# Kernel tuning notes

Measured on AMD Instinct MI355X. Metric: run time of the kernel, lower is better.

Reference implementation:

```python
import jax, jax.numpy as jnp
import numpy as np

N_DOC, N_WORD, N_ENT, N_POS = 10000, 20000, 10000, 60
D, D_POS_IN, D_WEMB = 128, 60, 300
E11, E22, E33, E01, E02, E03 = 320000, 160000, 3600, 300000, 100000, 150000
EPS = 1e-9


def spmm(rows, cols, vals, x, n_out):
    """Sparse (n_out x n_in) adjacency @ x via gather + weighted segment-sum."""
    return jax.ops.segment_sum(vals[:, None] * x[cols], rows, num_segments=n_out)


def gcn(rows, cols, vals, x, n_out, W=None, b=None):
    """GCN layer: adj @ (x W + b) with ReLU; identity=True in torch == W is None."""
    h = x if W is None else x @ W + b
    return jax.nn.relu(spmm(rows, cols, vals, h, n_out))


def setup_inputs():
    key = jax.random.key(0)
    ks = iter(jax.random.split(key, 64))
    randn = lambda s: jax.random.normal(next(ks), s, jnp.float32)
    rand = lambda s: jax.random.uniform(next(ks), s, dtype=jnp.float32)
    ridx = lambda s, hi: jax.random.randint(next(ks), s, 0, hi, jnp.int32)
    return {
        "f1": randn((N_WORD, D)),
        "f2": randn((N_ENT, D)),
        "f3": randn((N_POS, D_POS_IN)),
        "word_emb": randn((N_ENT, D_WEMB)),
        "a11_rows": ridx((E11,), N_WORD), "a11_cols": ridx((E11,), N_WORD), "a11_vals": rand((E11,)),
        "a22_rows": ridx((E22,), N_ENT), "a22_cols": ridx((E22,), N_ENT), "a22_vals": rand((E22,)),
        "a33_rows": ridx((E33,), N_POS), "a33_cols": ridx((E33,), N_POS), "a33_vals": rand((E33,)),
        "a01_rows": ridx((E01,), N_DOC), "a01_cols": ridx((E01,), N_WORD), "a01_vals": rand((E01,)),
        "a02_rows": ridx((E02,), N_DOC), "a02_cols": ridx((E02,), N_ENT), "a02_vals": rand((E02,)),
        "a03_rows": ridx((E03,), N_DOC), "a03_cols": ridx((E03,), N_POS), "a03_vals": rand((E03,)),
        "W3": randn((D_POS_IN, D)) * 0.1, "b3": jnp.zeros((D,), jnp.float32),
        "W1_2": randn((D, D)) * 0.1, "b1_2": jnp.zeros((D,), jnp.float32),
        "W2_2": randn((D, D)) * 0.1, "b2_2": jnp.zeros((D,), jnp.float32),
        "W3_2": randn((D, D)) * 0.1, "b3_2": jnp.zeros((D,), jnp.float32),
    }


def reference(f1, f2, f3, word_emb,
              a11_rows, a11_cols, a11_vals, a22_rows, a22_cols, a22_vals,
              a33_rows, a33_cols, a33_vals, a01_rows, a01_cols, a01_vals,
              a02_rows, a02_cols, a02_vals, a03_rows, a03_cols, a03_vals,
              W3, b3, W1_2, b1_2, W2_2, b2_2, W3_2, b3_2):
    # eval mode: F.dropout(training=False) is a no-op
    # type 1 (words): GCN(identity=True) -> GCN_2
    h1 = gcn(a11_rows, a11_cols, a11_vals, f1, N_WORD)
    h1 = gcn(a11_rows, a11_cols, a11_vals, h1, N_WORD, W1_2, b1_2)
    # type 2 (entities, concat_word_emb=True): GCN(identity=True) -> GCN_2 -> concat word_emb
    h2 = gcn(a22_rows, a22_cols, a22_vals, f2, N_ENT)
    h2 = gcn(a22_rows, a22_cols, a22_vals, h2, N_ENT, W2_2, b2_2)
    h2 = jnp.concatenate([h2, word_emb], axis=-1)  # [N_ENT, D + D_WEMB]
    # type 3 (POS): full GCN -> GCN_2
    h3 = gcn(a33_rows, a33_cols, a33_vals, f3, N_POS, W3, b3)
    h3 = gcn(a33_rows, a33_cols, a33_vals, h3, N_POS, W3_2, b3_2)
    # cross-type aggregation onto documents + L2 normalization
    outs = []
    for rows, cols, vals, h in ((a01_rows, a01_cols, a01_vals, h1),
                                (a02_rows, a02_cols, a02_vals, h2),
                                (a03_rows, a03_cols, a03_vals, h3)):
        agg = spmm(rows, cols, vals, h, N_DOC)  # [N_DOC, d]
        outs.append(agg / (jnp.linalg.norm(agg, axis=-1, keepdims=True) + EPS))
    return tuple(outs)
```

## Files before the change

kernel.cpp:

```cpp
#include <hip/hip_runtime.h>
#include <hip/hip_bf16.h>

typedef __hip_bfloat16 bf16;

#define N_DOC   10000
#define N_WORD  20000
#define N_ENT   10000
#define N_POS   60
#define DD      128
#define D_WEMB  300
#define E11     320000
#define E22     160000
#define E33     3600
#define E01     300000
#define E02     100000
#define E03     150000

#define ROFF11  0
#define ROFF22  20000
#define ROFF33  30000
#define ROFF01  30060
#define ROFF02  40060
#define ROFF03  50060
#define NROWS   60060
#define EOFF11  0
#define EOFF22  320000
#define EOFF33  480000
#define EOFF01  483600
#define EOFF02  783600
#define EOFF03  883600
#define NEDGES  1033600

#define BSHIFT  9
#define NBUCK   118
#define BCAP    18432
#define P1_TILE 4096
#define P1_EPT  8

#define BFO_F1B     0
#define BFO_F2B     1280000
#define BFO_WEMBB   1920000
#define BFO_E0B     3420000
#define BFO_S0B     4349952
#define BFO_S1B     5629952
#define BFO_E1B     6909952
#define BFO_P3A     7549952
#define BFO_P3B     7557632
#define BFO_INT     7565312

__device__ __forceinline__ float loadf(const void* p, size_t i, int isb) {
    return isb ? __bfloat162float(((const bf16*)p)[i])
               : ((const float*)p)[i];
}
__device__ __forceinline__ float b2f(unsigned u16) {
    union { unsigned v; float f; } x; x.v = u16 << 16; return x.f;
}
__device__ __forceinline__ unsigned f2b(float f) {
    bf16 h = __float2bfloat16(f);
    union { bf16 h; unsigned short u; } x; x.h = h; return (unsigned)x.u;
}
__device__ __forceinline__ void storef(void* p, size_t i, int asb, float v) {
    if (asb) ((unsigned short*)p)[i] = (unsigned short)f2b(v);
    else     ((float*)p)[i] = v;
}
__device__ __forceinline__ unsigned pack_pair(int col, float v) {
    return (f2b(v) << 16) | (unsigned)col;
}

__device__ __forceinline__ void edge_decode(
        int i,
        const int* __restrict__ r11, const int* __restrict__ c11, const void* __restrict__ v11,
        const int* __restrict__ r22, const int* __restrict__ c22, const void* __restrict__ v22,
        const int* __restrict__ r33, const int* __restrict__ c33, const void* __restrict__ v33,
        const int* __restrict__ r01, const int* __restrict__ c01, const void* __restrict__ v01,
        const int* __restrict__ r02, const int* __restrict__ c02, const void* __restrict__ v02,
        const int* __restrict__ r03, const int* __restrict__ c03, const void* __restrict__ v03,
        int isb, int& slot, int& col, float& val) {
    if      (i < EOFF22) { int k = i;          slot = ROFF11 + r11[k]; col = c11[k]; val = loadf(v11, k, isb); }
    else if (i < EOFF33) { int k = i - EOFF22; slot = ROFF22 + r22[k]; col = c22[k]; val = loadf(v22, k, isb); }
    else if (i < EOFF01) { int k = i - EOFF33; slot = ROFF33 + r33[k]; col = c33[k]; val = loadf(v33, k, isb); }
    else if (i < EOFF02) { int k = i - EOFF01; slot = ROFF01 + r01[k]; col = c01[k]; val = loadf(v01, k, isb); }
    else if (i < EOFF03) { int k = i - EOFF02; slot = ROFF02 + r02[k]; col = c02[k]; val = loadf(v02, k, isb); }
    else                 { int k = i - EOFF03; slot = ROFF03 + r03[k]; col = c03[k]; val = loadf(v03, k, isb); }
}

__global__ void detect_kernel(const unsigned* __restrict__ probe, int* __restrict__ flag,
                              int* __restrict__ bcur) {
    __shared__ int cnt;
    if (threadIdx.x == 0) cnt = 0;
    __syncthreads();
    int insane = 0;
    for (int i = threadIdx.x; i < 1024; i += 256) {
        float x = __uint_as_float(probe[i]);
        float a = fabsf(x);
        if (!(a > 1e-10f && a < 1e10f)) insane++;
    }
    atomicAdd(&cnt, insane);
    if (bcur && threadIdx.x < NBUCK) bcur[threadIdx.x] = threadIdx.x * BCAP;
    __syncthreads();
    if (threadIdx.x == 0) *flag = (cnt > 512) ? 1 : 0;
}

__device__ __forceinline__ void conv_seg(const void* __restrict__ src,
                                         unsigned* __restrict__ dst,
                                         int npairs, int isb, int tid, int stride) {
    if (isb) {
        const unsigned* s = (const unsigned*)src;
        for (int i = tid; i < npairs; i += stride) dst[i] = s[i];
    } else {
        const float2* s = (const float2*)src;
        for (int i = tid; i < npairs; i += stride) {
            float2 x = s[i];
            dst[i] = f2b(x.x) | (f2b(x.y) << 16);
        }
    }
}
__global__ void convert_bf16(const void* __restrict__ f1, const void* __restrict__ f2,
                             const void* __restrict__ wemb,
                             unsigned* __restrict__ f1b, unsigned* __restrict__ f2b,
                             unsigned* __restrict__ wembB,
                             const int* __restrict__ dflag) {
    int isb = *dflag;
    int tid = blockIdx.x * blockDim.x + threadIdx.x;
    int stride = gridDim.x * blockDim.x;
    conv_seg(f1,   f1b,   N_WORD * (DD / 2),     isb, tid, stride);
    conv_seg(f2,   f2b,   N_ENT  * (DD / 2),     isb, tid, stride);
    conv_seg(wemb, wembB, N_ENT  * (D_WEMB / 2), isb, tid, stride);
}

__global__ __launch_bounds__(512) void bin_edges(
        const int* __restrict__ r11, const int* __restrict__ c11, const void* __restrict__ v11,
        const int* __restrict__ r22, const int* __restrict__ c22, const void* __restrict__ v22,
        const int* __restrict__ r33, const int* __restrict__ c33, const void* __restrict__ v33,
        const int* __restrict__ r01, const int* __restrict__ c01, const void* __restrict__ v01,
        const int* __restrict__ r02, const int* __restrict__ c02, const void* __restrict__ v02,
        const int* __restrict__ r03, const int* __restrict__ c03, const void* __restrict__ v03,
        int* __restrict__ bcur, uint2* __restrict__ staging,
        const int* __restrict__ dflag) {
    __shared__ int hist[NBUCK], gbase[NBUCK], cursor[NBUCK];
    int t = threadIdx.x;
    if (t < NBUCK) { hist[t] = 0; cursor[t] = 0; }
    __syncthreads();
    int isb = *dflag;
    int base0 = blockIdx.x * P1_TILE;
    unsigned rx[P1_EPT], ry[P1_EPT];
    int bk[P1_EPT];
    #pragma unroll
    for (int k = 0; k < P1_EPT; ++k) {
        int i = base0 + t + k * 512;
        bk[k] = -1;
        if (i < NEDGES) {
            int slot, col; float val;
            edge_decode(i, r11, c11, v11, r22, c22, v22, r33, c33, v33,
                        r01, c01, v01, r02, c02, v02, r03, c03, v03,
                        isb, slot, col, val);
            rx[k] = ((unsigned)slot << 16) | (unsigned)col;
            ry[k] = f2b(val);
            bk[k] = slot >> BSHIFT;
            atomicAdd(&hist[bk[k]], 1);
        }
    }
    __syncthreads();
    if (t < NBUCK) {
        int c = hist[t];
        gbase[t] = c ? atomicAdd(bcur + t, c) : 0;
    }
    __syncthreads();
    #pragma unroll
    for (int k = 0; k < P1_EPT; ++k) {
        if (bk[k] >= 0) {
            int p = atomicAdd(&cursor[bk[k]], 1);
            int dst = gbase[bk[k]] + p;
            if (dst < (bk[k] + 1) * BCAP)
                staging[dst] = make_uint2(rx[k], ry[k]);
        }
    }
}

__global__ void scan_buckets(const int* __restrict__ bcur, int* __restrict__ bbase,
                             int* __restrict__ G) {
    __shared__ int wtop[2];
    int t = threadIdx.x;
    int cnt = 0;
    if (t < NBUCK) {
        int c = bcur[t] - t * BCAP;
        cnt = (c < BCAP) ? c : BCAP;
    }
    int lane = t & 63, w = t >> 6;
    int s = cnt;
    #pragma unroll
    for (int off = 1; off < 64; off <<= 1) {
        int y = __shfl_up(s, off);
        if (lane >= off) s += y;
    }
    if (lane == 63) wtop[w] = s;
    __syncthreads();
    int woff = (w > 0) ? wtop[0] : 0;
    if (t < NBUCK) bbase[t] = woff + s - cnt;
    if (t == NBUCK - 1) { bbase[NBUCK] = woff + s; G[NROWS] = woff + s; }
}

__global__ __launch_bounds__(512) void finalize_csr(
        const int* __restrict__ bcur, const int* __restrict__ bbase,
        const uint2* __restrict__ staging,
        int* __restrict__ G, unsigned* __restrict__ pairs) {
    __shared__ int h[512], rp[512], cu[512];
    __shared__ int wsum2[8];
    int b = blockIdx.x, t = threadIdx.x;
    int cnt = bcur[b] - b * BCAP;
    if (cnt > BCAP) cnt = BCAP;
    int bb = bbase[b];
    h[t] = 0;
    __syncthreads();
    const uint2* st = staging + (size_t)b * BCAP;
    for (int i = t; i < cnt; i += 512)
        atomicAdd(&h[(st[i].x >> 16) & 511], 1);
    __syncthreads();
    int lane = t & 63, w = t >> 6;
    int x = h[t];
    int s = x;
    #pragma unroll
    for (int off = 1; off < 64; off <<= 1) {
        int y = __shfl_up(s, off);
        if (lane >= off) s += y;
    }
    if (lane == 63) wsum2[w] = s;
    __syncthreads();
    if (t < 8) {
        int v = wsum2[t];
        #pragma unroll
        for (int off = 1; off < 8; off <<= 1) {
            int y = __shfl_up(v, off);
            if (lane >= off) v += y;
        }
        wsum2[t] = v;
    }
    __syncthreads();
    int myrp = ((w > 0) ? wsum2[w - 1] : 0) + s - x;
    rp[t] = myrp;
    cu[t] = 0;
    int slot = (b << BSHIFT) + t;
    if (slot < NROWS) G[slot] = bb + myrp;
    __syncthreads();
    for (int i = t; i < cnt; i += 512) {
        uint2 r = st[i];
        int sl = (r.x >> 16) & 511;
        int p = atomicAdd(&cu[sl], 1);
        pairs[bb + rp[sl] + p] = (r.y << 16) | (r.x & 0xffffu);
    }
}

__global__ void hist2_kernel(const int* __restrict__ rowsA, int nEA,
                             const int* __restrict__ rowsB, int nEB,
                             int nA, int* __restrict__ cnt) {
    int i = blockIdx.x * blockDim.x + threadIdx.x;
    if (i < nEA) atomicAdd(cnt + rowsA[i], 1);
    else if (i < nEA + nEB) atomicAdd(cnt + nA + rowsB[i - nEA], 1);
}

__device__ void scan_ex(const int* __restrict__ cnt, int* __restrict__ rp, int n) {
    __shared__ int wsum[16];
    __shared__ int carry;
    int t = threadIdx.x, lane = t & 63, w = t >> 6;
    if (t == 0) carry = 0;
    __syncthreads();
    for (int base = 0; base < n; base += 1024) {
        int i = base + t;
        int x = (i < n) ? cnt[i] : 0;
        int s = x;
        #pragma unroll
        for (int off = 1; off < 64; off <<= 1) {
            int y = __shfl_up(s, off);
            if (lane >= off) s += y;
        }
        if (lane == 63) wsum[w] = s;
        __syncthreads();
        if (w == 0) {
            int v = (lane < 16) ? wsum[lane] : 0;
            #pragma unroll
            for (int off = 1; off < 16; off <<= 1) {
                int y = __shfl_up(v, off);
                if (lane >= off) v += y;
            }
            if (lane < 16) wsum[lane] = v;
        }
        __syncthreads();
        int woff = (w > 0) ? wsum[w - 1] : 0;
        if (i < n) rp[i] = carry + woff + s - x;
        __syncthreads();
        if (t == 0) carry += wsum[15];
        __syncthreads();
    }
    if (t == 0) rp[n] = carry;
}

__global__ __launch_bounds__(1024) void scan2_kernel(
        const int* __restrict__ cntA, int* __restrict__ rpA, int nA,
        const int* __restrict__ cntB, int* __restrict__ rpB, int nB) {
    scan_ex(cntA, rpA, nA);
    __syncthreads();
    scan_ex(cntB, rpB, nB);
}

// ... 234 lines not shown
                int pi = lane + 64 * s;
                if (pi < P2) {
                    float2 x = s0p[pi], y = s1p[pi];
                    a2[s].x  = fmaf(v0, x.x, a2[s].x);
                    a2[s].y  = fmaf(v0, x.y, a2[s].y);
                    b2v[s].x = fmaf(v1, y.x, b2v[s].x);
                    b2v[s].y = fmaf(v1, y.y, b2v[s].y);
                }
            }
        }
    }
    if (e < e1) {
        unsigned pp = pairs[e];
        int c = pp & 0xffffu;
        float v = b2f(pp >> 16);
        float x0, x1;
        if (s1b) {
            unsigned u = ((const unsigned*)((const bf16*)src1 + (size_t)c * DD))[lane];
            x0 = b2f(u & 0xffffu); x1 = b2f(u >> 16);
        } else {
            float2 x = ((const float2*)((const float*)src1 + (size_t)c * DD))[lane];
            x0 = x.x; x1 = x.y;
        }
        x0 = fmaxf(x0, 0.f); x1 = fmaxf(x1, 0.f);
        a1.x = fmaf(v, x0, a1.x); a1.y = fmaf(v, x1, a1.y);
        if (s2b) {
            const unsigned* sp = (const unsigned*)((const bf16*)src2 + (size_t)c * D_WEMB);
            #pragma unroll
            for (int s = 0; s < 3; ++s) {
                int pi = lane + 64 * s;
                if (pi < P2) {
                    unsigned u = sp[pi];
                    a2[s].x = fmaf(v, b2f(u & 0xffffu), a2[s].x);
                    a2[s].y = fmaf(v, b2f(u >> 16),     a2[s].y);
                }
            }
        } else {
            const float2* sp = (const float2*)((const float*)src2 + (size_t)c * D_WEMB);
            #pragma unroll
            for (int s = 0; s < 3; ++s) {
                int pi = lane + 64 * s;
                if (pi < P2) {
                    float2 x = sp[pi];
                    a2[s].x = fmaf(v, x.x, a2[s].x);
                    a2[s].y = fmaf(v, x.y, a2[s].y);
                }
            }
        }
    }
    float t1x = a1.x + b1.x, t1y = a1.y + b1.y;
    float t2x[3], t2y[3];
    #pragma unroll
    for (int s = 0; s < 3; ++s) { t2x[s] = a2[s].x + b2v[s].x; t2y[s] = a2[s].y + b2v[s].y; }
    float ss = t1x * t1x + t1y * t1y;
    #pragma unroll
    for (int s = 0; s < 3; ++s) {
        int pi = lane + 64 * s;
        if (pi < P2) ss += t2x[s] * t2x[s] + t2y[s] * t2y[s];
    }
    #pragma unroll
    for (int off = 32; off > 0; off >>= 1) ss += __shfl_down(ss, off);
    ss = __shfl(ss, 0);
    float inv = 1.0f / (sqrtf(ss) + 1e-9f);
    size_t base = elem_off + (size_t)row * (DD + D_WEMB);
    if (isb) {
        ((unsigned*)((bf16*)out + base))[lane] = f2b(t1x * inv) | (f2b(t1y * inv) << 16);
        unsigned* o2 = (unsigned*)((bf16*)out + base + DD);
        #pragma unroll
        for (int s = 0; s < 3; ++s) {
            int pi = lane + 64 * s;
            if (pi < P2) o2[pi] = f2b(t2x[s] * inv) | (f2b(t2y[s] * inv) << 16);
        }
    } else {
        ((float2*)((float*)out + base))[lane] = make_float2(t1x * inv, t1y * inv);
        float2* o2 = (float2*)((float*)out + base + DD);
        #pragma unroll
        for (int s = 0; s < 3; ++s) {
            int pi = lane + 64 * s;
            if (pi < P2) o2[pi] = make_float2(t2x[s] * inv, t2y[s] * inv);
        }
    }
}

template<bool RELU, int K>
__device__ __forceinline__ void rowpar_body256(
        const void* __restrict__ X, int xisb,
        const void* __restrict__ W, const void* __restrict__ b,
        void* __restrict__ out, int oisb, int isb,
        int row, int tid, float* xr ) {
    int half = tid >> 7;
    int j = tid & 127;
    float* xrh = xr + half * K;
    if (j < K) {
        float x = loadf(X, (size_t)row * K + j, xisb);
        if (RELU) x = fmaxf(x, 0.f);
        xrh[j] = x;
    }
    __syncthreads();
    float acc = loadf(b, j, isb);
    #pragma unroll 8
    for (int k = 0; k < K; ++k)
        acc = fmaf(xrh[k], loadf(W, (size_t)k * 128 + j, isb), acc);
    storef(out, (size_t)row * 128 + j, oisb, acc);
}

template<bool RELU>
__global__ void spmm_gather128(const int* __restrict__ rowptr, const unsigned* __restrict__ pairs,
                               const void* __restrict__ src, int src_flagged,
                               void* __restrict__ dst, int dst_flagged,
                               int n, const int* __restrict__ dflag) {
    int row = blockIdx.x * 4 + (threadIdx.x >> 6);
    if (row >= n) return;
    int isb = *dflag;
    gather128_body<RELU>(rowptr, pairs, src, src_flagged ? isb : 0,
                         dst, dst_flagged ? isb : 0, row, threadIdx.x & 63);
}

template<int KP, bool PRELU>
__global__ void hop_pos(const int* __restrict__ G, const unsigned* __restrict__ pairs,
                        int roff1, const void* __restrict__ src1, void* __restrict__ dst1, int n1, int B1,
                        int roff2, const void* __restrict__ src2, void* __restrict__ dst2, int n2, int B2,
                        const void* __restrict__ PX, const void* __restrict__ PW,
                        const void* __restrict__ Pb, void* __restrict__ PO,
                        const int* __restrict__ dflag) {
    __shared__ float xr[2 * KP];
    int b = blockIdx.x;
    if (b < B1) {
        int row = b * 4 + (threadIdx.x >> 6);
        if (row >= n1) return;
        gather128_body<false>(G + roff1, pairs, src1, 1, dst1, 1, row, threadIdx.x & 63);
    } else if (b < B1 + B2) {
        int row = (b - B1) * 4 + (threadIdx.x >> 6);
        if (row >= n2) return;
        gather128_body<false>(G + roff2, pairs, src2, 1, dst2, 1, row, threadIdx.x & 63);
    } else {
        int isb = *dflag;
        int row = (b - B1 - B2) * 2 + (threadIdx.x >> 7);
        if (row >= N_POS) return;
        rowpar_body256<PRELU, KP>(PX, isb, PW, Pb, PO, isb, isb, row, threadIdx.x, xr);
    }
}

template<bool RELU>
__global__ void spmm_norm128(const int* __restrict__ rowptr, const unsigned* __restrict__ pairs,
                             const void* __restrict__ src, int src_flagged,
                             void* __restrict__ out, size_t elem_off,
                             int n, const int* __restrict__ dflag) {
    int row = blockIdx.x * 4 + (threadIdx.x >> 6);
    if (row >= n) return;
    int isb = *dflag;
    norm128_body<RELU>(rowptr, pairs, src, src_flagged ? isb : 0, out, elem_off,
                       row, threadIdx.x & 63, isb);
}

__global__ void spmm2_norm(const int* __restrict__ rowptr, const unsigned* __restrict__ pairs,
                           const void* __restrict__ src1, int s1_flagged,
                           const void* __restrict__ src2, int s2_flagged,
                           void* __restrict__ out, size_t elem_off,
                           int n, const int* __restrict__ dflag) {
    int row = blockIdx.x * 4 + (threadIdx.x >> 6);
    if (row >= n) return;
    int isb = *dflag;
    norm428_body(rowptr, pairs, src1, s1_flagged ? isb : 0, src2, s2_flagged ? isb : 0,
                 out, elem_off, row, threadIdx.x & 63, isb);
}

__global__ void final_norm_all(const int* __restrict__ G, const unsigned* __restrict__ pairs,
                               const void* __restrict__ s1, const void* __restrict__ e0b,
                               const void* __restrict__ wemb, const void* __restrict__ p3b,
                               void* __restrict__ out,
                               size_t off1, size_t off2, size_t off3,
                               const int* __restrict__ dflag) {
    int isb = *dflag;
    int lane = threadIdx.x & 63;
    int b = blockIdx.x;
    if (b < 2500) {
        int row = b * 4 + (threadIdx.x >> 6);
        if (row >= N_DOC) return;
        norm128_body<true>(G + ROFF01, pairs, s1, 1, out, off1, row, lane, isb);
    } else if (b < 5000) {
        int row = (b - 2500) * 4 + (threadIdx.x >> 6);
        if (row >= N_DOC) return;
        norm428_body(G + ROFF02, pairs, e0b, 1, wemb, 1, out, off2, row, lane, isb);
    } else {
        int row = (b - 5000) * 4 + (threadIdx.x >> 6);
        if (row >= N_DOC) return;
        norm128_body<true>(G + ROFF03, pairs, p3b, isb, out, off3, row, lane, isb);
    }
}

template<bool RELU>
__global__ void spmm_kernel(const int* __restrict__ rows, const int* __restrict__ cols,
                            const void* __restrict__ vals,
                            const void* __restrict__ src, int sstride, int src_flagged,
                            float* __restrict__ dst, int dstride, int doff,
                            int d, int nE, const int* __restrict__ dflag) {
    int e = blockIdx.x * (blockDim.x >> 6) + (threadIdx.x >> 6);
    if (e >= nE) return;
    int isb  = *dflag;
    int sisb = src_flagged ? isb : 0;
    int lane = threadIdx.x & 63;
    int r = rows[e];
    int c = cols[e];
    float v = loadf(vals, e, isb);
    size_t sbase = (size_t)c * sstride;
    float* dp = dst + (size_t)r * dstride + doff;
    if (sisb) {
        const unsigned* sp = (const unsigned*)((const bf16*)src + sbase);
        for (int j = 2 * lane; j < d; j += 128) {
            unsigned u = sp[j >> 1];
            float x0 = b2f(u & 0xffffu);
            float x1 = b2f(u >> 16);
            if (RELU) { x0 = fmaxf(x0, 0.f); x1 = fmaxf(x1, 0.f); }
            atomicAdd(dp + j,     v * x0);
            atomicAdd(dp + j + 1, v * x1);
        }
    } else {
        const float2* sp = (const float2*)((const float*)src + sbase);
        for (int j = 2 * lane; j < d; j += 128) {
            float2 x = sp[j >> 1];
            if (RELU) { x.x = fmaxf(x.x, 0.f); x.y = fmaxf(x.y, 0.f); }
            atomicAdd(dp + j,     v * x.x);
// ... 17 lines not shown
            int k = vidx >> 4, jl4 = vidx & 15;
            uint2 u = Wg[k * 32 + (jc >> 2) + jl4];
            float4 vv;
            vv.x = b2f(u.x & 0xffffu);
            vv.y = b2f(u.x >> 16);
            vv.z = b2f(u.y & 0xffffu);
            vv.w = b2f(u.y >> 16);
            Wl4[vidx] = vv;
        }
    } else {
        const float4* Wg = (const float4*)W;
        float4* Wl4 = (float4*)Wl;
        for (int vidx = tid; vidx < 2048; vidx += 256) {
            int k = vidx >> 4, jl4 = vidx & 15;
            Wl4[vidx] = Wg[k * 32 + (jc >> 2) + jl4];
        }
    }
    __syncthreads();
    int j2 = tid & 31;
    int g  = tid >> 5;
    float bc0 = loadf(b, jc + 2 * j2, isb);
    float bc1 = loadf(b, jc + 2 * j2 + 1, isb);
    int i0 = bx * 64 + g * 8;
    float a0[8], a1[8];
    #pragma unroll
    for (int r = 0; r < 8; ++r) { a0[r] = bc0; a1[r] = bc1; }
    const char* xbase = (const char*)X + (size_t)i0 * 128 * (XB ? 2 : 4);
    const float2* Wl2 = (const float2*)Wl;
    #pragma unroll 2
    for (int k4 = 0; k4 < 32; ++k4) {
        float2 w0 = Wl2[(4 * k4 + 0) * 32 + j2];
        float2 w1 = Wl2[(4 * k4 + 1) * 32 + j2];
        float2 w2 = Wl2[(4 * k4 + 2) * 32 + j2];
        float2 w3 = Wl2[(4 * k4 + 3) * 32 + j2];
        #pragma unroll
        for (int r = 0; r < 8; ++r) {
            float4 v;
            if (XB) {
                uint2 u = ((const uint2*)xbase)[r * 32 + k4];
                v.x = b2f(u.x & 0xffffu); v.y = b2f(u.x >> 16);
                v.z = b2f(u.y & 0xffffu); v.w = b2f(u.y >> 16);
            } else {
                v = ((const float4*)xbase)[r * 32 + k4];
            }
            if (RELU) {
                v.x = fmaxf(v.x, 0.f); v.y = fmaxf(v.y, 0.f);
                v.z = fmaxf(v.z, 0.f); v.w = fmaxf(v.w, 0.f);
            }
            a0[r] = fmaf(v.w, w3.x, fmaf(v.z, w2.x, fmaf(v.y, w1.x, fmaf(v.x, w0.x, a0[r]))));
            a1[r] = fmaf(v.w, w3.y, fmaf(v.z, w2.y, fmaf(v.y, w1.y, fmaf(v.x, w0.y, a1[r]))));
        }
    }
    #pragma unroll
    for (int r = 0; r < 8; ++r) {
        int i = i0 + r;
        if (i < n) {
            if (oisb) {
                ((unsigned*)((bf16*)out + (size_t)i * 128 + jc))[j2] =
                    f2b(a0[r]) | (f2b(a1[r]) << 16);
            } else {
                ((float2*)((float*)out + (size_t)i * 128 + jc))[j2] =
                    make_float2(a0[r], a1[r]);
            }
        }
    }
}

template<bool RELU>
__global__ __launch_bounds__(256) void gemm_tile(
        const float* __restrict__ X, const void* __restrict__ W,
        const void* __restrict__ b, void* __restrict__ out, int n,
        const int* __restrict__ dflag) {
    __shared__ float Wl[128 * 64];
    int isb = *dflag;
    gemm_tile_body<RELU, false>(X, W, b, out, n, blockIdx.x, blockIdx.y, isb, isb, Wl);
}

template<bool RELU>
__global__ __launch_bounds__(256) void gemm_tile_b2g(
        const void* __restrict__ X1, const void* __restrict__ W1, const void* __restrict__ b1,
        void* __restrict__ out1, int n1, int G1,
        const void* __restrict__ X2, const void* __restrict__ W2, const void* __restrict__ b2,
        void* __restrict__ out2, int n2, int GT,
        const int* __restrict__ G33, const unsigned* __restrict__ pairs,
        const void* __restrict__ P3a, void* __restrict__ P3b,
        const int* __restrict__ dflag) {
    __shared__ float Wl[128 * 64];
    int isb = *dflag;
    int x = blockIdx.x;
    if (x < G1) {
        gemm_tile_body<RELU, true>(X1, W1, b1, out1, n1, x, blockIdx.y, isb, 1, Wl);
    } else if (x < GT) {
        gemm_tile_body<RELU, true>(X2, W2, b2, out2, n2, x - G1, blockIdx.y, isb, 1, Wl);
    } else {
        if (blockIdx.y != 0) return;
        int row = (x - GT) * 4 + (threadIdx.x >> 6);
        if (row >= N_POS) return;
        gather128_body<false>(G33, pairs, P3a, isb, P3b, isb, row, threadIdx.x & 63);
    }
}

template<bool RELU>
__global__ __launch_bounds__(256) void gemm128_kernel(
        const float* __restrict__ X, const void* __restrict__ W,
        const void* __restrict__ b, float* __restrict__ out, int n,
        const int* __restrict__ dflag) {
    __shared__ float Wl[128 * 128];
    int isb = *dflag;
    int tid = threadIdx.x;
    if (isb) {
        const uint2* Wg = (const uint2*)W;
        float4* Wl4 = (float4*)Wl;
        for (int idx = tid; idx < 4096; idx += 256) {
            uint2 u = Wg[idx];
            float4 vv;
            vv.x = b2f(u.x & 0xffffu);
            vv.y = b2f(u.x >> 16);
            vv.z = b2f(u.y & 0xffffu);
            vv.w = b2f(u.y >> 16);
            Wl4[idx] = vv;
        }
    } else {
        const float4* Wg = (const float4*)W;
        float4* Wl4 = (float4*)Wl;
        for (int idx = tid; idx < 4096; idx += 256) Wl4[idx] = Wg[idx];
    }
    __syncthreads();
    int j = tid & 127;
    int h = tid >> 7;
    float bj = loadf(b, j, isb);
    int row0 = blockIdx.x * 64 + h * 32;
    for (int q = 0; q < 8; ++q) {
        int gi = row0 + q * 4;
        if (gi >= n) break;
        const float4* x0 = (const float4*)(X + (size_t)gi * 128);
        const float4* x1 = x0 + 32;
        const float4* x2 = x1 + 32;
        const float4* x3 = x2 + 32;
        float a0 = bj, a1 = bj, a2 = bj, a3 = bj;
        #pragma unroll 4
        for (int k4 = 0; k4 < 32; ++k4) {
            float4 v0 = x0[k4], v1 = x1[k4], v2 = x2[k4], v3 = x3[k4];
            if (RELU) {
                v0.x = fmaxf(v0.x, 0.f); v0.y = fmaxf(v0.y, 0.f); v0.z = fmaxf(v0.z, 0.f); v0.w = fmaxf(v0.w, 0.f);
                v1.x = fmaxf(v1.x, 0.f); v1.y = fmaxf(v1.y, 0.f); v1.z = fmaxf(v1.z, 0.f); v1.w = fmaxf(v1.w, 0.f);
                v2.x = fmaxf(v2.x, 0.f); v2.y = fmaxf(v2.y, 0.f); v2.z = fmaxf(v2.z, 0.f); v2.w = fmaxf(v2.w, 0.f);
                v3.x = fmaxf(v3.x, 0.f); v3.y = fmaxf(v3.y, 0.f); v3.z = fmaxf(v3.z, 0.f); v3.w = fmaxf(v3.w, 0.f);
            }
            float w0 = Wl[(4 * k4 + 0) * 128 + j];
            float w1 = Wl[(4 * k4 + 1) * 128 + j];
            float w2 = Wl[(4 * k4 + 2) * 128 + j];
            float w3 = Wl[(4 * k4 + 3) * 128 + j];
            a0 = fmaf(v0.w, w3, fmaf(v0.z, w2, fmaf(v0.y, w1, fmaf(v0.x, w0, a0))));
            a1 = fmaf(v1.w, w3, fmaf(v1.z, w2, fmaf(v1.y, w1, fmaf(v1.x, w0, a1))));
            a2 = fmaf(v2.w, w3, fmaf(v2.z, w2, fmaf(v2.y, w1, fmaf(v2.x, w0, a2))));
            a3 = fmaf(v3.w, w3, fmaf(v3.z, w2, fmaf(v3.y, w1, fmaf(v3.x, w0, a3))));
        }
        float* o = out + (size_t)gi * 128 + j;
        o[0] = a0; o[128] = a1; o[256] = a2; o[384] = a3;
    }
}

template<bool RELU, int K>
__global__ void rowpar_gemm(const void* __restrict__ X, int x_flagged,
                            const void* __restrict__ W, const void* __restrict__ b,
                            void* __restrict__ out, int out_flagged,
                            const int* __restrict__ dflag) {
    __shared__ float xr[K];
    int isb  = *dflag;
    int xisb = x_flagged ? isb : 0;
    int oisb = out_flagged ? isb : 0;
    int row = blockIdx.x;
    int j = threadIdx.x;
    if (j < K) {
        float x = loadf(X, (size_t)row * K + j, xisb);
        if (RELU) x = fmaxf(x, 0.f);
        xr[j] = x;
    }
    __syncthreads();
    float acc = loadf(b, j, isb);
    #pragma unroll 8
// ... 56 lines not shown
        ss += x.x * x.x + x.y * x.y;
    }
    #pragma unroll
    for (int off = 32; off > 0; off >>= 1) ss += __shfl_down(ss, off);
    ss = __shfl(ss, 0);
    float inv = 1.0f / (sqrtf(ss) + 1e-9f);
    size_t bbase = elem_off + (size_t)row * d;
    if (isb) {
        unsigned* o = (unsigned*)((bf16*)out + bbase);
        for (int j = 2 * lane; j < d; j += 128) {
            float2 x = a2[j >> 1];
            o[j >> 1] = f2b(x.x * inv) | (f2b(x.y * inv) << 16);
        }
    } else {
        float2* o = (float2*)((float*)out + bbase);
        for (int j = 2 * lane; j < d; j += 128) {
            float2 x = a2[j >> 1];
            o[j >> 1] = make_float2(x.x * inv, x.y * inv);
        }
    }
}

static inline int spmm_grid(int nE) { return (nE + 3) / 4; }
static inline int row_grid(int n)   { return (n + 3) / 4; }
static inline int pad8(int x)       { return (x + 7) & ~7; }

static void build2(hipStream_t stream,
                   const int* rowsA, const int* colsA, const void* valsA, int nA, int nEA,
                   const int* rowsB, const int* colsB, const void* valsB, int nB, int nEB,
                   int* rpA, int* rpB, int* curAB, unsigned* pairsA, unsigned* pairsB,
                   const int* dflag) {
    int nE = nEA + nEB;
    hipMemsetAsync(curAB, 0, (size_t)(nA + nB) * 4, stream);
    hist2_kernel<<<(nE + 255) / 256, 256, 0, stream>>>(rowsA, nEA, rowsB, nEB, nA, curAB);
    scan2_kernel<<<1, 1024, 0, stream>>>(curAB, rpA, nA, curAB + nA, rpB, nB);
    copy2_kernel<<<(nA + nB + 255) / 256, 256, 0, stream>>>(rpA, rpB, nA, nB, curAB);
    scatter2_kernel<<<(nE + 255) / 256, 256, 0, stream>>>(
        rowsA, colsA, valsA, nEA, rowsB, colsB, valsB, nEB, nA, curAB, pairsA, pairsB, dflag);
}

extern "C" void kernel_launch(void* const* d_in, const int* in_sizes, int n_in,
                              void* d_out, int out_size, void* d_ws, size_t ws_size,
                              hipStream_t stream) {
    const void* f1   = d_in[0];
    const void* f2   = d_in[1];
    const void* f3   = d_in[2];
    const void* wemb = d_in[3];
    const int*  a11r = (const int*)d_in[4];
    const int*  a11c = (const int*)d_in[5];
    const void* a11v = d_in[6];
    const int*  a22r = (const int*)d_in[7];
    const int*  a22c = (const int*)d_in[8];
    const void* a22v = d_in[9];
    const int*  a33r = (const int*)d_in[10];
    const int*  a33c = (const int*)d_in[11];
    const void* a33v = d_in[12];
    const int*  a01r = (const int*)d_in[13];
    const int*  a01c = (const int*)d_in[14];
    const void* a01v = d_in[15];
    const int*  a02r = (const int*)d_in[16];
    const int*  a02c = (const int*)d_in[17];
    const void* a02v = d_in[18];
    const int*  a03r = (const int*)d_in[19];
    const int*  a03c = (const int*)d_in[20];
    const void* a03v = d_in[21];
    const void* W3   = d_in[22];
    const void* b3   = d_in[23];
    const void* W1_2 = d_in[24];
    const void* b1_2 = d_in[25];
    const void* W2_2 = d_in[26];
    const void* b2_2 = d_in[27];
    const void* W3_2 = d_in[28];
    const void* b3_2 = d_in[29];

    int*   dflag = (int*)d_ws;
    float* base  = (float*)d_ws + 16;

    const size_t OUT1_OFF = 0;
    const size_t OUT2_OFF = (size_t)N_DOC * DD;
    const size_t OUT3_OFF = OUT2_OFF + (size_t)N_DOC * (DD + D_WEMB);

    dim3 blk(256);

    const size_t BIG_INTS = (size_t)(NROWS + 1) + 128 + 132 + NEDGES;
    const size_t WS_BIG = 64 + ((size_t)BFO_INT + BIG_INTS) * 4;
    const size_t WS_MID = 64 + 22240000ull + (60008ull + 620000ull) * 4;

    if (ws_size >= WS_BIG) {
        uint2* staging = (uint2*)base;
        void*  f1b   = (void*)(base + BFO_F1B);
        void*  f2b   = (void*)(base + BFO_F2B);
        void*  wembB = (void*)(base + BFO_WEMBB);
        void*  E0b   = (void*)(base + BFO_E0B);
        void*  S0b   = (void*)(base + BFO_S0B);
        void*  S1b   = (void*)(base + BFO_S1B);
        void*  E1b   = (void*)(base + BFO_E1B);
        float* P3a   = base + BFO_P3A;
        float* P3b   = base + BFO_P3B;
        int*   G     = (int*)(base + BFO_INT);
        int*   bcur  = G + (NROWS + 1);
        int*   bbase = bcur + 128;
        unsigned* pairs = (unsigned*)(bbase + 132);

        detect_kernel<<<1, 256, 0, stream>>>((const unsigned*)f1, dflag, bcur);

        const int NB1 = (NEDGES + P1_TILE - 1) / P1_TILE;
        bin_edges<<<NB1, 512, 0, stream>>>(
            a11r, a11c, a11v, a22r, a22c, a22v, a33r, a33c, a33v,
            a01r, a01c, a01v, a02r, a02c, a02v, a03r, a03c, a03v,
            bcur, staging, dflag);
        scan_buckets<<<1, 128, 0, stream>>>(bcur, bbase, G);
        finalize_csr<<<NBUCK, 512, 0, stream>>>(bcur, bbase, staging, G, pairs);

        convert_bf16<<<2048, 256, 0, stream>>>(
            f1, f2, wemb, (unsigned*)f1b, (unsigned*)f2b, (unsigned*)wembB, dflag);

        int B1 = row_grid(N_WORD), B2 = row_grid(N_ENT);
        hop_pos<60, false><<<B1 + B2 + 30, blk, 0, stream>>>(
            G, pairs, ROFF11, f1b, S0b, N_WORD, B1,
            ROFF22, f2b, E0b, N_ENT, B2,
            f3, W3, b3, P3a, dflag);
        {
            int G1 = pad8((N_WORD + 63) / 64), G2 = pad8((N_ENT + 63) / 64);
            int GT = G1 + G2;
            gemm_tile_b2g<true><<<dim3(GT + row_grid(N_POS), 2), 256, 0, stream>>>(
                S0b, W1_2, b1_2, S1b, N_WORD, G1,
                E0b, W2_2, b2_2, E1b, N_ENT, GT,
                G + ROFF33, pairs, P3a, P3b, dflag);
        }
        hop_pos<128, true><<<B1 + B2 + 30, blk, 0, stream>>>(
            G, pairs, ROFF11, S1b, S0b, N_WORD, B1,
            ROFF22, E1b, E0b, N_ENT, B2,
            P3b, W3_2, b3_2, P3a, dflag);
        spmm_gather128<false><<<row_grid(N_POS), blk, 0, stream>>>(
            G + ROFF33, pairs, P3a, 1, P3b, 1, N_POS, dflag);

        final_norm_all<<<7500, blk, 0, stream>>>(
            G, pairs, S0b, E0b, wembB, P3b, d_out, OUT1_OFF, OUT2_OFF, OUT3_OFF, dflag);
    } else if (ws_size >= WS_MID) {
        detect_kernel<<<1, 256, 0, stream>>>((const unsigned*)f1, dflag, (int*)nullptr);
        float* S0   = base;
        float* S1   = base + 2560000;
        float* E0   = base;
        float* E1   = base + 1280000;
        float* P3a  = base;
        float* P3b  = base + 7680;
        int* I = (int*)(base + 5560000);
        {
            int* rpA = I; int* rpB = rpA + (N_WORD + 1); int* cur = rpB + (N_DOC + 1);
            unsigned* pA = (unsigned*)(cur + N_WORD + N_DOC); unsigned* pB = pA + E11;
            build2(stream, a11r, a11c, a11v, N_WORD, E11,
                   a01r, a01c, a01v, N_DOC, E01, rpA, rpB, cur, pA, pB, dflag);
            spmm_gather128<false><<<row_grid(N_WORD), blk, 0, stream>>>(
                rpA, pA, f1, 1, S0, 0, N_WORD, dflag);
            gemm_tile<true><<<dim3(pad8((N_WORD + 63) / 64), 2), 256, 0, stream>>>(
                S0, W1_2, b1_2, S1, N_WORD, dflag);
            spmm_gather128<false><<<row_grid(N_WORD), blk, 0, stream>>>(
                rpA, pA, S1, 1, S0, 1, N_WORD, dflag);
            spmm_norm128<true><<<row_grid(N_DOC), blk, 0, stream>>>(
                rpB, pB, S0, 1, d_out, OUT1_OFF, N_DOC, dflag);
        }
        {
            int* rpA = I; int* rpB = rpA + (N_ENT + 1); int* cur = rpB + (N_DOC + 1);
            unsigned* pA = (unsigned*)(cur + N_ENT + N_DOC); unsigned* pB = pA + E22;
            build2(stream, a22r, a22c, a22v, N_ENT, E22,
                   a02r, a02c, a02v, N_DOC, E02, rpA, rpB, cur, pA, pB, dflag);
            spmm_gather128<false><<<row_grid(N_ENT), blk, 0, stream>>>(
                rpA, pA, f2, 1, E0, 0, N_ENT, dflag);
            gemm_tile<true><<<dim3(pad8((N_ENT + 63) / 64), 2), 256, 0, stream>>>(
                E0, W2_2, b2_2, E1, N_ENT, dflag);
            spmm_gather128<false><<<row_grid(N_ENT), blk, 0, stream>>>(
                rpA, pA, E1, 1, E0, 1, N_ENT, dflag);
            spmm2_norm<<<row_grid(N_DOC), blk, 0, stream>>>(
                rpB, pB, E0, 1, wemb, 1, d_out, OUT2_OFF, N_DOC, dflag);
        }
        {
            int* rpA = I; int* rpB = rpA + (N_POS + 1); int* cur = rpB + (N_DOC + 1);
            unsigned* pA = (unsigned*)(cur + N_POS + N_DOC); unsigned* pB = pA + E33;
            build2(stream, a33r, a33c, a33v, N_POS, E33,
                   a03r, a03c, a03v, N_DOC, E03, rpA, rpB, cur, pA, pB, dflag);
            rowpar_gemm<false, 60><<<N_POS, 128, 0, stream>>>(
                f3, 1, W3, b3, P3a, 1, dflag);
            spmm_gather128<false><<<row_grid(N_POS), blk, 0, stream>>>(
                rpA, pA, P3a, 1, P3b, 1, N_POS, dflag);
            rowpar_gemm<true, 128><<<N_POS, 128, 0, stream>>>(
                P3b, 1, W3_2, b3_2, P3a, 1, dflag);
            spmm_gather128<false><<<row_grid(N_POS), blk, 0, stream>>>(
                rpA, pA, P3a, 1, P3b, 1, N_POS, dflag);
            spmm_norm128<true><<<row_grid(N_DOC), blk, 0, stream>>>(
                rpB, pB, P3b, 1, d_out, OUT3_OFF, N_DOC, dflag);
        }
    } else {
        detect_kernel<<<1, 256, 0, stream>>>((const unsigned*)f1, dflag, (int*)nullptr);
        float* S0   = base;
        float* S1   = base + 2560000;
        float* AGG1 = S1;
        float* E0   = base;
        float* E1   = base + 1280000;
        float* AGG2 = base + 1280000;
        float* P3a  = base;
        float* P3b  = base + 7680;
        float* AGG3 = base + 15360;
        hipMemsetAsync(S0, 0, (size_t)N_WORD * DD * 4, stream);
        spmm_kernel<false><<<spmm_grid(E11), blk, 0, stream>>>(
            a11r, a11c, a11v, f1, DD, 1, S0, DD, 0, DD, E11, dflag);
        gemm128_kernel<true><<<(N_WORD + 63) / 64, 256, 0, stream>>>(
            S0, W1_2, b1_2, S1, N_WORD, dflag);
        hipMemsetAsync(S0, 0, (size_t)N_WORD * DD * 4, stream);
        spmm_kernel<false><<<spmm_grid(E11), blk, 0, stream>>>(
            a11r, a11c, a11v, S1, DD, 0, S0, DD, 0, DD, E11, dflag);
        hipMemsetAsync(AGG1, 0, (size_t)N_DOC * DD * 4, stream);
        spmm_kernel<true><<<spmm_grid(E01), blk, 0, stream>>>(
            a01r, a01c, a01v, S0, DD, 0, AGG1, DD, 0, DD, E01, dflag);
        l2norm_kernel<<<row_grid(N_DOC), blk, 0, stream>>>(
            AGG1, DD, d_out, OUT1_OFF, N_DOC, dflag);

        hipMemsetAsync(E0, 0, (size_t)N_ENT * DD * 4, stream);
        spmm_kernel<false><<<spmm_grid(E22), blk, 0, stream>>>(
            a22r, a22c, a22v, f2, DD, 1, E0, DD, 0, DD, E22, dflag);
        gemm128_kernel<true><<<(N_ENT + 63) / 64, 256, 0, stream>>>(
            E0, W2_2, b2_2, E1, N_ENT, dflag);
// ... 28 lines not shown
```

Measured before the change: 294.2 us.

## Fuse binning, bf16 conversion and POS linear into one launch; fold scan into finalize

```diff
diff --git a/kernel.cpp b/kernel.cpp
--- a/kernel.cpp
+++ b/kernel.cpp
@@ -36,17 +36,24 @@
 #define BCAP    18432
 #define P1_TILE 4096
 #define P1_EPT  8
-
-#define BFO_F1B     0
-#define BFO_F2B     1280000
-#define BFO_WEMBB   1920000
-#define BFO_E0B     3420000
-#define BFO_S0B     4349952
-#define BFO_S1B     5629952
-#define BFO_E1B     6909952
-#define BFO_P3A     7549952
-#define BFO_P3B     7557632
-#define BFO_INT     7565312
+#define NB1K    253
+#define NCONV   120
+#define NPOSB1  15
+
+#define HFO_STAGE   0
+#define HFO_PAIRS   4349952
+#define HFO_G       5383552
+#define HFO_BCUR    5443616
+#define HFO_F1B     5443744
+#define HFO_F2B     6723744
+#define HFO_WEMBB   7363744
+#define HFO_S0B     8863744
+#define HFO_S1B     10143744
+#define HFO_E0B     11423744
+#define HFO_E1B     12063744
+#define HFO_P3A     12703744
+#define HFO_P3B     12711424
+#define HFO_END     12719104
 
 __device__ __forceinline__ float loadf(const void* p, size_t i, int isb) {
     return isb ? __bfloat162float(((const bf16*)p)[i])
@@ -115,20 +122,54 @@
         }
     }
 }
-__global__ void convert_bf16(const void* __restrict__ f1, const void* __restrict__ f2,
-                             const void* __restrict__ wemb,
-                             unsigned* __restrict__ f1b, unsigned* __restrict__ f2b,
-                             unsigned* __restrict__ wembB,
-                             const int* __restrict__ dflag) {
-    int isb = *dflag;
-    int tid = blockIdx.x * blockDim.x + threadIdx.x;
-    int stride = gridDim.x * blockDim.x;
-    conv_seg(f1,   f1b,   N_WORD * (DD / 2),     isb, tid, stride);
-    conv_seg(f2,   f2b,   N_ENT  * (DD / 2),     isb, tid, stride);
-    conv_seg(wemb, wembB, N_ENT  * (D_WEMB / 2), isb, tid, stride);
-}
-
-__global__ __launch_bounds__(512) void bin_edges(
+
+template<bool RELU, int K>
+__device__ __forceinline__ void rowpar_body256(
+        const void* __restrict__ X, int xisb,
+        const void* __restrict__ W, const void* __restrict__ b,
+        void* __restrict__ out, int oisb, int isb,
+        int row, int tid, float* xr ) {
+    int half = tid >> 7;
+    int j = tid & 127;
+    float* xrh = xr + half * K;
+    if (j < K) {
+        float x = loadf(X, (size_t)row * K + j, xisb);
+        if (RELU) x = fmaxf(x, 0.f);
+        xrh[j] = x;
+    }
+    __syncthreads();
+    float acc = loadf(b, j, isb);
+    #pragma unroll 8
+    for (int k = 0; k < K; ++k)
+        acc = fmaf(xrh[k], loadf(W, (size_t)k * 128 + j, isb), acc);
+    storef(out, (size_t)row * 128 + j, oisb, acc);
+}
+
+template<bool RELU, int K>
+__device__ __forceinline__ void rowpar_body512(
+        const void* __restrict__ X, int xisb,
+        const void* __restrict__ W, const void* __restrict__ b,
+        void* __restrict__ out, int oisb, int isb,
+        int row0, int tid, float* xr ) {
+    int q = tid >> 7;
+    int j = tid & 127;
+    int row = row0 + q;
+    float* xrh = xr + q * K;
+    if (row < N_POS && j < K) {
+        float x = loadf(X, (size_t)row * K + j, xisb);
+        if (RELU) x = fmaxf(x, 0.f);
+        xrh[j] = x;
+    }
+    __syncthreads();
+    if (row >= N_POS) return;
+    float acc = loadf(b, j, isb);
+    #pragma unroll 8
+    for (int k = 0; k < K; ++k)
+        acc = fmaf(xrh[k], loadf(W, (size_t)k * 128 + j, isb), acc);
+    storef(out, (size_t)row * 128 + j, oisb, acc);
+}
+
+__global__ __launch_bounds__(512) void bin_edges_fused(
         const int* __restrict__ r11, const int* __restrict__ c11, const void* __restrict__ v11,
         const int* __restrict__ r22, const int* __restrict__ c22, const void* __restrict__ v22,
         const int* __restrict__ r33, const int* __restrict__ c33, const void* __restrict__ v33,
@@ -136,89 +177,106 @@
         const int* __restrict__ r02, const int* __restrict__ c02, const void* __restrict__ v02,
         const int* __restrict__ r03, const int* __restrict__ c03, const void* __restrict__ v03,
         int* __restrict__ bcur, uint2* __restrict__ staging,
+        const void* __restrict__ f1, const void* __restrict__ f2, const void* __restrict__ wemb,
+        unsigned* __restrict__ f1q, unsigned* __restrict__ f2q, unsigned* __restrict__ wq,
+        const void* __restrict__ f3, const void* __restrict__ W3, const void* __restrict__ b3,
+        void* __restrict__ P3a,
         const int* __restrict__ dflag) {
-    __shared__ int hist[NBUCK], gbase[NBUCK], cursor[NBUCK];
+    __shared__ int smem_i[3 * NBUCK];
+    int* hist   = smem_i;
+    int* gbase  = smem_i + NBUCK;
+    int* cursor = smem_i + 2 * NBUCK;
+    int blk = blockIdx.x;
     int t = threadIdx.x;
-    if (t < NBUCK) { hist[t] = 0; cursor[t] = 0; }
-    __syncthreads();
-    int isb = *dflag;
-    int base0 = blockIdx.x * P1_TILE;
-    unsigned rx[P1_EPT], ry[P1_EPT];
-    int bk[P1_EPT];
-    #pragma unroll
-    for (int k = 0; k < P1_EPT; ++k) {
-        int i = base0 + t + k * 512;
-        bk[k] = -1;
-        if (i < NEDGES) {
-            int slot, col; float val;
-            edge_decode(i, r11, c11, v11, r22, c22, v22, r33, c33, v33,
-                        r01, c01, v01, r02, c02, v02, r03, c03, v03,
-                        isb, slot, col, val);
-            rx[k] = ((unsigned)slot << 16) | (unsigned)col;
-            ry[k] = f2b(val);
-            bk[k] = slot >> BSHIFT;
-            atomicAdd(&hist[bk[k]], 1);
-        }
-    }
-    __syncthreads();
-    if (t < NBUCK) {
-        int c = hist[t];
-        gbase[t] = c ? atomicAdd(bcur + t, c) : 0;
-    }
-    __syncthreads();
-    #pragma unroll
-    for (int k = 0; k < P1_EPT; ++k) {
-        if (bk[k] >= 0) {
-            int p = atomicAdd(&cursor[bk[k]], 1);
-            int dst = gbase[bk[k]] + p;
-            if (dst < (bk[k] + 1) * BCAP)
-                staging[dst] = make_uint2(rx[k], ry[k]);
-        }
-    }
-}
-
-__global__ void scan_buckets(const int* __restrict__ bcur, int* __restrict__ bbase,
-                             int* __restrict__ G) {
-    __shared__ int wtop[2];
-    int t = threadIdx.x;
-    int cnt = 0;
+    if (blk < NB1K) {
+        if (t < NBUCK) { hist[t] = 0; cursor[t] = 0; }
+        __syncthreads();
+        int isb = *dflag;
+        int base0 = blk * P1_TILE;
+        unsigned rx[P1_EPT], ry[P1_EPT];
+        int bk[P1_EPT];
+        #pragma unroll
+        for (int k = 0; k < P1_EPT; ++k) {
+            int i = base0 + t + k * 512;
+            bk[k] = -1;
+            if (i < NEDGES) {
+                int slot, col; float val;
+                edge_decode(i, r11, c11, v11, r22, c22, v22, r33, c33, v33,
+                            r01, c01, v01, r02, c02, v02, r03, c03, v03,
+                            isb, slot, col, val);
+                rx[k] = ((unsigned)slot << 16) | (unsigned)col;
+                ry[k] = f2b(val);
+                bk[k] = slot >> BSHIFT;
+                atomicAdd(&hist[bk[k]], 1);
+            }
+        }
+        __syncthreads();
+        if (t < NBUCK) {
+            int c = hist[t];
+            gbase[t] = c ? atomicAdd(bcur + t, c) : 0;
+        }
+        __syncthreads();
+        #pragma unroll
+        for (int k = 0; k < P1_EPT; ++k) {
+            if (bk[k] >= 0) {
+                int p = atomicAdd(&cursor[bk[k]], 1);
+                int dst = gbase[bk[k]] + p;
+                if (dst < (bk[k] + 1) * BCAP)
+                    staging[dst] = make_uint2(rx[k], ry[k]);
+            }
+        }
+    } else if (blk < NB1K + NCONV) {
+        int isb = *dflag;
+        int tid = (blk - NB1K) * 512 + t;
+        int stride = NCONV * 512;
+        conv_seg(f1,   f1q, N_WORD * (DD / 2),     isb, tid, stride);
+        conv_seg(f2,   f2q, N_ENT  * (DD / 2),     isb, tid, stride);
+        conv_seg(wemb, wq,  N_ENT  * (D_WEMB / 2), isb, tid, stride);
+    } else {
+        int isb = *dflag;
+        int row0 = (blk - NB1K - NCONV) * 4;
+        rowpar_body512<false, 60>(f3, isb, W3, b3, P3a, isb, isb, row0, t, (float*)smem_i);
+    }
+}
+
+__global__ __launch_bounds__(512) void finalize_csr(
+        const int* __restrict__ bcur, const uint2* __restrict__ staging,
+        int* __restrict__ G, unsigned* __restrict__ pairs) {
+    __shared__ int h[512], rp[512], cu[512];
+    __shared__ int wsum2[8], wtop[2], bbs[2];
+    int b = blockIdx.x, t = threadIdx.x;
+    int lane = t & 63, w = t >> 6;
+    h[t] = 0;
+    int cnt_t = 0, s = 0;
     if (t < NBUCK) {
         int c = bcur[t] - t * BCAP;
-        cnt = (c < BCAP) ? c : BCAP;
-    }
-    int lane = t & 63, w = t >> 6;
-    int s = cnt;
-    #pragma unroll
-    for (int off = 1; off < 64; off <<= 1) {
-        int y = __shfl_up(s, off);
-        if (lane >= off) s += y;
-    }
-    if (lane == 63) wtop[w] = s;
-    __syncthreads();
-    int woff = (w > 0) ? wtop[0] : 0;
-    if (t < NBUCK) bbase[t] = woff + s - cnt;
-    if (t == NBUCK - 1) { bbase[NBUCK] = woff + s; G[NROWS] = woff + s; }
-}
-
-__global__ __launch_bounds__(512) void finalize_csr(
-        const int* __restrict__ bcur, const int* __restrict__ bbase,
-        const uint2* __restrict__ staging,
-        int* __restrict__ G, unsigned* __restrict__ pairs) {
-    __shared__ int h[512], rp[512], cu[512];
-    __shared__ int wsum2[8];
-    int b = blockIdx.x, t = threadIdx.x;
-    int cnt = bcur[b] - b * BCAP;
-    if (cnt > BCAP) cnt = BCAP;
-    int bb = bbase[b];
-    h[t] = 0;
-    __syncthreads();
+        cnt_t = (c < BCAP) ? c : BCAP;
+    }
+    if (t < 128) {
+        s = cnt_t;
+        #pragma unroll
+        for (int off = 1; off < 64; off <<= 1) {
+            int y = __shfl_up(s, off);
+            if (lane >= off) s += y;
+        }
+        if (lane == 63) wtop[w] = s;
+    }
+    __syncthreads();
+    if (t == b) {
+        bbs[0] = ((w > 0) ? wtop[0] : 0) + s - cnt_t;
+        bbs[1] = cnt_t;
+    }
+    if (b == NBUCK - 1 && t == NBUCK - 1)
+        G[NROWS] = ((w > 0) ? wtop[0] : 0) + s;
+    __syncthreads();
+    int bb = bbs[0];
+    int cnt = bbs[1];
     const uint2* st = staging + (size_t)b * BCAP;
     for (int i = t; i < cnt; i += 512)
         atomicAdd(&h[(st[i].x >> 16) & 511], 1);
     __syncthreads();
-    int lane = t & 63, w = t >> 6;
     int x = h[t];
-    int s = x;
+    s = x;
     #pragma unroll
     for (int off = 1; off < 64; off <<= 1) {
         int y = __shfl_up(s, off);
@@ -619,28 +677,6 @@
     }
 }
 
-template<bool RELU, int K>
-__device__ __forceinline__ void rowpar_body256(
-        const void* __restrict__ X, int xisb,
-        const void* __restrict__ W, const void* __restrict__ b,
-        void* __restrict__ out, int oisb, int isb,
-        int row, int tid, float* xr ) {
-    int half = tid >> 7;
-    int j = tid & 127;
-    float* xrh = xr + half * K;
-    if (j < K) {
-        float x = loadf(X, (size_t)row * K + j, xisb);
-        if (RELU) x = fmaxf(x, 0.f);
-        xrh[j] = x;
-    }
-    __syncthreads();
-    float acc = loadf(b, j, isb);
-    #pragma unroll 8
-    for (int k = 0; k < K; ++k)
-        acc = fmaf(xrh[k], loadf(W, (size_t)k * 128 + j, isb), acc);
-    storef(out, (size_t)row * 128 + j, oisb, acc);
-}
-
 template<bool RELU>
 __global__ void spmm_gather128(const int* __restrict__ rowptr, const unsigned* __restrict__ pairs,
                                const void* __restrict__ src, int src_flagged,
@@ -653,28 +689,26 @@
                          dst, dst_flagged ? isb : 0, row, threadIdx.x & 63);
 }
 
-template<int KP, bool PRELU>
-__global__ void hop_pos(const int* __restrict__ G, const unsigned* __restrict__ pairs,
-                        int roff1, const void* __restrict__ src1, void* __restrict__ dst1, int n1, int B1,
-                        int roff2, const void* __restrict__ src2, void* __restrict__ dst2, int n2, int B2,
-                        const void* __restrict__ PX, const void* __restrict__ PW,
-                        const void* __restrict__ Pb, void* __restrict__ PO,
-                        const int* __restrict__ dflag) {
-    __shared__ float xr[2 * KP];
+__global__ void hop_posg(const int* __restrict__ G, const unsigned* __restrict__ pairs,
+                         int roff1, const void* __restrict__ src1, void* __restrict__ dst1, int n1, int B1,
+                         int roff2, const void* __restrict__ src2, void* __restrict__ dst2, int n2, int B2,
+                         const void* __restrict__ Psrc, void* __restrict__ Pdst,
+                         const int* __restrict__ dflag) {
     int b = blockIdx.x;
+    int lane = threadIdx.x & 63;
     if (b < B1) {
         int row = b * 4 + (threadIdx.x >> 6);
         if (row >= n1) return;
-        gather128_body<false>(G + roff1, pairs, src1, 1, dst1, 1, row, threadIdx.x & 63);
+        gather128_body<false>(G + roff1, pairs, src1, 1, dst1, 1, row, lane);
     } else if (b < B1 + B2) {
         int row = (b - B1) * 4 + (threadIdx.x >> 6);
         if (row >= n2) return;
-        gather128_body<false>(G + roff2, pairs, src2, 1, dst2, 1, row, threadIdx.x & 63);
+        gather128_body<false>(G + roff2, pairs, src2, 1, dst2, 1, row, lane);
     } else {
         int isb = *dflag;
-        int row = (b - B1 - B2) * 2 + (threadIdx.x >> 7);
+        int row = (b - B1 - B2) * 4 + (threadIdx.x >> 6);
         if (row >= N_POS) return;
-        rowpar_body256<PRELU, KP>(PX, isb, PW, Pb, PO, isb, isb, row, threadIdx.x, xr);
+        gather128_body<false>(G + ROFF33, pairs, Psrc, isb, Pdst, isb, row, lane);
     }
 }
 
@@ -858,8 +892,8 @@
         void* __restrict__ out1, int n1, int G1,
         const void* __restrict__ X2, const void* __restrict__ W2, const void* __restrict__ b2,
         void* __restrict__ out2, int n2, int GT,
-        const int* __restrict__ G33, const unsigned* __restrict__ pairs,
-        const void* __restrict__ P3a, void* __restrict__ P3b,
+        const void* __restrict__ PX, const void* __restrict__ PW,
+        const void* __restrict__ Pb, void* __restrict__ PO,
         const int* __restrict__ dflag) {
     __shared__ float Wl[128 * 64];
     int isb = *dflag;
@@ -870,9 +904,8 @@
         gemm_tile_body<RELU, true>(X2, W2, b2, out2, n2, x - G1, blockIdx.y, isb, 1, Wl);
     } else {
         if (blockIdx.y != 0) return;
-        int row = (x - GT) * 4 + (threadIdx.x >> 6);
-        if (row >= N_POS) return;
-        gather128_body<false>(G33, pairs, P3a, isb, P3b, isb, row, threadIdx.x & 63);
+        int row = (x - GT) * 2 + (threadIdx.x >> 7);
+        rowpar_body256<true, 128>(PX, isb, PW, Pb, PO, isb, isb, row, threadIdx.x, Wl);
     }
 }
 
@@ -1095,61 +1128,53 @@
 
     dim3 blk(256);
 
-    const size_t BIG_INTS = (size_t)(NROWS + 1) + 128 + 132 + NEDGES;
-    const size_t WS_BIG = 64 + ((size_t)BFO_INT + BIG_INTS) * 4;
+    const size_t WS_BIG = 64 + (size_t)HFO_END * 4;
     const size_t WS_MID = 64 + 22240000ull + (60008ull + 620000ull) * 4;
 
     if (ws_size >= WS_BIG) {
-        uint2* staging = (uint2*)base;
-        void*  f1b   = (void*)(base + BFO_F1B);
-        void*  f2b   = (void*)(base + BFO_F2B);
-        void*  wembB = (void*)(base + BFO_WEMBB);
-        void*  E0b   = (void*)(base + BFO_E0B);
-        void*  S0b   = (void*)(base + BFO_S0B);
-        void*  S1b   = (void*)(base + BFO_S1B);
-        void*  E1b   = (void*)(base + BFO_E1B);
-        float* P3a   = base + BFO_P3A;
-        float* P3b   = base + BFO_P3B;
-        int*   G     = (int*)(base + BFO_INT);
-        int*   bcur  = G + (NROWS + 1);
-        int*   bbase = bcur + 128;
-        unsigned* pairs = (unsigned*)(bbase + 132);
+        uint2*    staging = (uint2*)(base + HFO_STAGE);
+        unsigned* pairs   = (unsigned*)(base + HFO_PAIRS);
+        int*      G       = (int*)(base + HFO_G);
+        int*      bcur    = (int*)(base + HFO_BCUR);
+        void*     f1q     = (void*)(base + HFO_F1B);
+        void*     f2q     = (void*)(base + HFO_F2B);
+        void*     wq      = (void*)(base + HFO_WEMBB);
+        void*     S0b     = (void*)(base + HFO_S0B);
+        void*     S1b     = (void*)(base + HFO_S1B);
+        void*     E0b     = (void*)(base + HFO_E0B);
+        void*     E1b     = (void*)(base + HFO_E1B);
+        float*    P3a     = base + HFO_P3A;
+        float*    P3b     = base + HFO_P3B;
 
         detect_kernel<<<1, 256, 0, stream>>>((const unsigned*)f1, dflag, bcur);
 
-        const int NB1 = (NEDGES + P1_TILE - 1) / P1_TILE;
-        bin_edges<<<NB1, 512, 0, stream>>>(
+        bin_edges_fused<<<NB1K + NCONV + NPOSB1, 512, 0, stream>>>(
             a11r, a11c, a11v, a22r, a22c, a22v, a33r, a33c, a33v,
             a01r, a01c, a01v, a02r, a02c, a02v, a03r, a03c, a03v,
-            bcur, staging, dflag);
-        scan_buckets<<<1, 128, 0, stream>>>(bcur, bbase, G);
-        finalize_csr<<<NBUCK, 512, 0, stream>>>(bcur, bbase, staging, G, pairs);
-
-        convert_bf16<<<2048, 256, 0, stream>>>(
-            f1, f2, wemb, (unsigned*)f1b, (unsigned*)f2b, (unsigned*)wembB, dflag);
+            bcur, staging,
+            f1, f2, wemb, (unsigned*)f1q, (unsigned*)f2q, (unsigned*)wq,
+            f3, W3, b3, P3a, dflag);
+
+        finalize_csr<<<NBUCK, 512, 0, stream>>>(bcur, staging, G, pairs);
 
         int B1 = row_grid(N_WORD), B2 = row_grid(N_ENT);
-        hop_pos<60, false><<<B1 + B2 + 30, blk, 0, stream>>>(
-            G, pairs, ROFF11, f1b, S0b, N_WORD, B1,
-            ROFF22, f2b, E0b, N_ENT, B2,
-            f3, W3, b3, P3a, dflag);
+        hop_posg<<<B1 + B2 + row_grid(N_POS), blk, 0, stream>>>(
+            G, pairs, ROFF11, f1q, S0b, N_WORD, B1,
+            ROFF22, f2q, E0b, N_ENT, B2, P3a, P3b, dflag);
         {
             int G1 = pad8((N_WORD + 63) / 64), G2 = pad8((N_ENT + 63) / 64);
             int GT = G1 + G2;
-            gemm_tile_b2g<true><<<dim3(GT + row_grid(N_POS), 2), 256, 0, stream>>>(
+            gemm_tile_b2g<true><<<dim3(GT + 30, 2), 256, 0, stream>>>(
                 S0b, W1_2, b1_2, S1b, N_WORD, G1,
                 E0b, W2_2, b2_2, E1b, N_ENT, GT,
-                G + ROFF33, pairs, P3a, P3b, dflag);
-        }
-        hop_pos<128, true><<<B1 + B2 + 30, blk, 0, stream>>>(
+                P3b, W3_2, b3_2, P3a, dflag);
+        }
+        hop_posg<<<B1 + B2 + row_grid(N_POS), blk, 0, stream>>>(
             G, pairs, ROFF11, S1b, S0b, N_WORD, B1,
-            ROFF22, E1b, E0b, N_ENT, B2,
-            P3b, W3_2, b3_2, P3a, dflag);
-        spmm_gather128<false><<<row_grid(N_POS), blk, 0, stream>>>(
-            G + ROFF33, pairs, P3a, 1, P3b, 1, N_POS, dflag);
+            ROFF22, E1b, E0b, N_ENT, B2, P3a, P3b, dflag);
 
         final_norm_all<<<7500, blk, 0, stream>>>(
-            G, pairs, S0b, E0b, wembB, P3b, d_out, OUT1_OFF, OUT2_OFF, OUT3_OFF, dflag);
+            G, pairs, S0b, E0b, wq, P3b, d_out, OUT1_OFF, OUT2_OFF, OUT3_OFF, dflag);
     } else if (ws_size >= WS_MID) {
         detect_kernel<<<1, 256, 0, stream>>>((const unsigned*)f1, dflag, (int*)nullptr);
         float* S0   = base;
```

New measurement: 286.8 us. -2.5%, faster.
